# Kernel tuning notes

Measured on AMD Instinct MI355X. Metric: run time of the kernel, lower is better.

## Reference

```python
import jax, jax.numpy as jnp
import numpy as np

N, FEATURES, CODES, PAGES = 32768, 768, 64, 8192
BETA = 0.25


def _normalise(x):
    return x / jnp.linalg.norm(x, axis=-1, keepdims=True)


def setup_inputs() -> dict:
    key = jax.random.key(0)
    k_z, k_wi, k_wo, k_cb = jax.random.split(key, 4)
    return {
        "z": jax.random.normal(k_z, (N, FEATURES), dtype=jnp.float32),
        "w_in": jax.random.normal(k_wi, (CODES, FEATURES), dtype=jnp.float32) * 0.02,
        "b_in": jnp.zeros((CODES,), dtype=jnp.float32),
        "w_out": jax.random.normal(k_wo, (FEATURES, CODES), dtype=jnp.float32) * 0.02,
        "b_out": jnp.zeros((FEATURES,), dtype=jnp.float32),
        "codebook": jax.random.normal(k_cb, (PAGES, CODES), dtype=jnp.float32),
    }


def reference(z, w_in, b_in, w_out, b_out, codebook):
    sg = jax.lax.stop_gradient
    # project + L2-normalise samples and codes
    zq = _normalise(z @ w_in.T + b_in)          # [n, codes]
    cn = _normalise(codebook)                   # [pages, codes]
    # squared euclidean distance without materialising [n, pages, codes]:
    # ||z||^2 + ||c||^2 - 2 z c^T
    d = (
        jnp.sum(zq * zq, axis=-1, keepdims=True)
        + jnp.sum(cn * cn, axis=-1)[None, :]
        - 2.0 * (zq @ cn.T)
    )                                           # [n, pages]
    idxes = jnp.argmin(d, axis=-1)              # [n]
    codes = _normalise(codebook[idxes])         # lookup then normalise, as in source
    loss = BETA * jnp.mean((sg(zq) - codes) ** 2) + jnp.mean((zq - sg(codes)) ** 2)
    codes = zq + sg(codes - zq)                 # straight-through
    out = codes @ w_out.T + b_out               # [n, features]
    return out, loss, idxes
```

## Files before the change

### kernel.cpp

```cpp
#include <hip/hip_runtime.h>

#define N 32768
#define F 768
#define C 64
#define P 8192
#define TAU 1e-3f

typedef __attribute__((ext_vector_type(8))) short short8;
typedef __attribute__((ext_vector_type(4))) float f32x4;

#define WS_CNT    0
#define WS_CC     (WS_CNT + C*P)
#define WS_ZQT    (WS_CC + P)
#define WS_CODEST (WS_ZQT + C*N)
#define WS_IDX    (WS_CODEST + C*N)
#define WS_QN     (WS_IDX + N)
#define WS_ACC    (WS_QN + 1)
#define WS_QLIST  (WS_ACC + 1)
#define WS_CNH    ((WS_QLIST + N + 3) & ~3)
#define WS_CNL    (WS_CNH + (C*P)/2)
#define WS_ZQH    (WS_CNL + (C*P)/2)
#define WS_ZQL    (WS_ZQH + (C*N)/2)
#define WS_D12    (WS_ZQL + (C*N)/2)

#define OUT_LOSS_OFF (N*F)
#define OUT_IDX_OFF  (N*F + 1)

__device__ inline unsigned short f2bf(float x) {
    union { float f; unsigned u; } v; v.f = x;
    unsigned r = v.u + 0x7fffu + ((v.u >> 16) & 1u);
    return (unsigned short)(r >> 16);
}
__device__ inline float bf2f(unsigned short b) {
    union { unsigned u; float f; } v; v.u = ((unsigned)b) << 16;
    return v.f;
}

__global__ __launch_bounds__(256) void k1_norm_codebook(
    const float* __restrict__ cb, float* __restrict__ cnT, float* __restrict__ cc,
    unsigned short* __restrict__ cnh, unsigned short* __restrict__ cnl) {
    int p = blockIdx.x * 256 + threadIdx.x;
    const float4* cb4 = (const float4*)(cb + (size_t)p * C);
    float4 v[16];
    float ss = 0.f;
#pragma unroll
    for (int i = 0; i < 16; ++i) {
        v[i] = cb4[i];
        ss += v[i].x * v[i].x + v[i].y * v[i].y + v[i].z * v[i].z + v[i].w * v[i].w;
    }
    float nrm = sqrtf(ss);
    float s2 = 0.f;
    unsigned short hb[64], lb[64];
#pragma unroll
    for (int i = 0; i < 16; ++i) {
        float c4[4] = {v[i].x / nrm, v[i].y / nrm, v[i].z / nrm, v[i].w / nrm};
#pragma unroll
        for (int j = 0; j < 4; ++j) {
            cnT[(size_t)(i * 4 + j) * P + p] = c4[j];
            s2 += c4[j] * c4[j];
            unsigned short h = f2bf(c4[j]);
            hb[i * 4 + j] = h;
            lb[i * 4 + j] = f2bf(c4[j] - bf2f(h));
        }
    }
    cc[p] = s2;
#pragma unroll
    for (int i = 0; i < 8; ++i) {
        uint4 hv, lv;
        hv.x = (unsigned)hb[i*8+0] | ((unsigned)hb[i*8+1] << 16);
        hv.y = (unsigned)hb[i*8+2] | ((unsigned)hb[i*8+3] << 16);
        hv.z = (unsigned)hb[i*8+4] | ((unsigned)hb[i*8+5] << 16);
        hv.w = (unsigned)hb[i*8+6] | ((unsigned)hb[i*8+7] << 16);
        lv.x = (unsigned)lb[i*8+0] | ((unsigned)lb[i*8+1] << 16);
        lv.y = (unsigned)lb[i*8+2] | ((unsigned)lb[i*8+3] << 16);
        lv.z = (unsigned)lb[i*8+4] | ((unsigned)lb[i*8+5] << 16);
        lv.w = (unsigned)lb[i*8+6] | ((unsigned)lb[i*8+7] << 16);
        *(uint4*)&cnh[(size_t)p * 64 + i * 8] = hv;
        *(uint4*)&cnl[(size_t)p * 64 + i * 8] = lv;
    }
}

__global__ __launch_bounds__(256) void k2_project(
    const float* __restrict__ z, const float* __restrict__ w_in, const float* __restrict__ b_in,
    float* __restrict__ zqT, unsigned short* __restrict__ zqh, unsigned short* __restrict__ zql) {
    __shared__ float zrow[128 * 33];
    __shared__ float wrow[64 * 32];
    __shared__ float red[128 * 9];
    int tid = threadIdx.x;
    int tr = tid & 31;
    int tc = tid >> 5;
    int rb = blockIdx.x * 128;

    float y[4][8];
#pragma unroll
    for (int i = 0; i < 4; ++i)
#pragma unroll
        for (int j = 0; j < 8; ++j) y[i][j] = 0.f;

    for (int kt = 0; kt < F; kt += 32) {
        __syncthreads();
        for (int i = tid; i < 128 * 32; i += 256) {
            int r = i >> 5, k = i & 31;
            zrow[r * 33 + k] = z[(size_t)(rb + r) * F + kt + k];
        }
        for (int i = tid; i < 64 * 32; i += 256) {
            int c = i >> 5, k = i & 31;
            wrow[c * 32 + k] = w_in[(size_t)c * F + kt + k];
        }
        __syncthreads();
#pragma unroll
        for (int k4 = 0; k4 < 8; ++k4) {
            float zs[4][4];
#pragma unroll
            for (int i = 0; i < 4; ++i)
#pragma unroll
                for (int kk = 0; kk < 4; ++kk)
                    zs[i][kk] = zrow[(tr * 4 + i) * 33 + k4 * 4 + kk];
#pragma unroll
            for (int j = 0; j < 8; ++j) {
                float4 wv = *(const float4*)&wrow[(tc * 8 + j) * 32 + k4 * 4];
#pragma unroll
                for (int i = 0; i < 4; ++i)
                    y[i][j] = fmaf(zs[i][3], wv.w,
                              fmaf(zs[i][2], wv.z,
                              fmaf(zs[i][1], wv.y,
                              fmaf(zs[i][0], wv.x, y[i][j]))));
            }
        }
    }
#pragma unroll
    for (int j = 0; j < 8; ++j) {
        float b = b_in[tc * 8 + j];
#pragma unroll
        for (int i = 0; i < 4; ++i) y[i][j] += b;
    }
    __syncthreads();
#pragma unroll
    for (int i = 0; i < 4; ++i) {
        float s = 0.f;
#pragma unroll
        for (int j = 0; j < 8; ++j) s += y[i][j] * y[i][j];
        red[(tr * 4 + i) * 9 + tc] = s;
    }
    __syncthreads();
    float nrm[4];
#pragma unroll
    for (int i = 0; i < 4; ++i) {
        float t = 0.f;
#pragma unroll
        for (int t8 = 0; t8 < 8; ++t8) t += red[(tr * 4 + i) * 9 + t8];
        nrm[i] = sqrtf(t);
    }
    float q[4][8];
#pragma unroll
    for (int i = 0; i < 4; ++i)
#pragma unroll
        for (int j = 0; j < 8; ++j) q[i][j] = y[i][j] / nrm[i];
#pragma unroll
    for (int j = 0; j < 8; ++j) {
        int c = tc * 8 + j;
        float4 o = make_float4(q[0][j], q[1][j], q[2][j], q[3][j]);
        *(float4*)&zqT[(size_t)c * N + rb + tr * 4] = o;
    }
#pragma unroll
    for (int i = 0; i < 4; ++i) {
        unsigned short h[8], l[8];
#pragma unroll
        for (int j = 0; j < 8; ++j) {
            h[j] = f2bf(q[i][j]);
            l[j] = f2bf(q[i][j] - bf2f(h[j]));
        }
        uint4 hv, lv;
        hv.x = (unsigned)h[0] | ((unsigned)h[1] << 16);
        hv.y = (unsigned)h[2] | ((unsigned)h[3] << 16);
        hv.z = (unsigned)h[4] | ((unsigned)h[5] << 16);
        hv.w = (unsigned)h[6] | ((unsigned)h[7] << 16);
        lv.x = (unsigned)l[0] | ((unsigned)l[1] << 16);
        lv.y = (unsigned)l[2] | ((unsigned)l[3] << 16);
        lv.z = (unsigned)l[4] | ((unsigned)l[5] << 16);
        lv.w = (unsigned)l[6] | ((unsigned)l[7] << 16);
        size_t ro = (size_t)(rb + tr * 4 + i) * 64 + tc * 8;
        *(uint4*)&zqh[ro] = hv;
        *(uint4*)&zql[ro] = lv;
    }
}

__global__ __launch_bounds__(256, 4) void k3_argmin_mfma(
    const unsigned short* __restrict__ zqh, const unsigned short* __restrict__ zql,
    const unsigned short* __restrict__ cnh, const unsigned short* __restrict__ cnl,
    float4* __restrict__ d12) {
    __shared__ unsigned short lfrag[8 * 4 * 64 * 8];
    int tid = threadIdx.x;
    int w = tid >> 6, lane = tid & 63;
    int col = lane & 15, quad = lane >> 4;
    int rb = (blockIdx.x & 255) * 128;
    int ph = blockIdx.x >> 8;
    int wrow = rb + w * 32;
    int p0 = ph * (P / 4);

    short8 ah[2][2], al[2][2];
#pragma unroll
    for (int mm = 0; mm < 2; ++mm)
#pragma unroll
        for (int kf = 0; kf < 2; ++kf) {
            size_t off = (size_t)(wrow + mm * 16 + col) * 64 + kf * 32 + quad * 8;
            ah[mm][kf] = *(const short8*)&zqh[off];
            al[mm][kf] = *(const short8*)&zql[off];
        }

    float s1[8], s2[8]; int i1[8];
#pragma unroll
    for (int r = 0; r < 8; ++r) { s1[r] = -3.4e38f; s2[r] = -3.4e38f; i1[r] = 0; }

    int sq = (tid >> 4) & 3, scol = tid & 15, sf = w;
    const unsigned short* ssrc = (sf & 2) ? cnl : cnh;
    int skf = sf & 1;

    for (int pt = p0; pt < p0 + P / 4; pt += 128) {
        __syncthreads();
#pragma unroll
        for (int nt = 0; nt < 8; ++nt) {
            int p = pt + nt * 16 + scol;
            uint4 dv = *(const uint4*)&ssrc[(size_t)p * 64 + skf * 32 + sq * 8];
            *(uint4*)&lfrag[((nt * 4 + sf) * 64 + (tid & 63)) * 8] = dv;
        }
        __syncthreads();
#pragma unroll 2
        for (int nt = 0; nt < 8; ++nt) {
            short8 bh0 = *(const short8*)&lfrag[((nt * 4 + 0) * 64 + lane) * 8];
            short8 bh1 = *(const short8*)&lfrag[((nt * 4 + 1) * 64 + lane) * 8];
            short8 bl0 = *(const short8*)&lfrag[((nt * 4 + 2) * 64 + lane) * 8];
            short8 bl1 = *(const short8*)&lfrag[((nt * 4 + 3) * 64 + lane) * 8];
            int p = pt + nt * 16 + col;
#pragma unroll
            for (int mm = 0; mm < 2; ++mm) {
                f32x4 acc = {0.f, 0.f, 0.f, 0.f};
                acc = __builtin_amdgcn_mfma_f32_16x16x32_bf16(ah[mm][0], bh0, acc, 0, 0, 0);
                acc = __builtin_amdgcn_mfma_f32_16x16x32_bf16(ah[mm][1], bh1, acc, 0, 0, 0);
                acc = __builtin_amdgcn_mfma_f32_16x16x32_bf16(ah[mm][0], bl0, acc, 0, 0, 0);
                acc = __builtin_amdgcn_mfma_f32_16x16x32_bf16(ah[mm][1], bl1, acc, 0, 0, 0);
                acc = __builtin_amdgcn_mfma_f32_16x16x32_bf16(al[mm][0], bh0, acc, 0, 0, 0);
                acc = __builtin_amdgcn_mfma_f32_16x16x32_bf16(al[mm][1], bh1, acc, 0, 0, 0);
#pragma unroll
                for (int s = 0; s < 4; ++s) {
                    float sv = acc[s];
                    int r = mm * 4 + s;
                    bool gt = sv > s1[r];
                    i1[r] = gt ? p : i1[r];
                    s2[r] = fmaxf(s2[r], fminf(s1[r], sv));
                    s1[r] = fmaxf(s1[r], sv);
                }
            }
        }
    }
#pragma unroll
    for (int r = 0; r < 8; ++r) {
        float a1v = s1[r], a2v = s2[r]; int ai = i1[r];
#pragma unroll
        for (int m = 1; m <= 8; m <<= 1) {
            float b1 = __shfl_xor(a1v, m); int bi = __shfl_xor(ai, m);
            float b2 = __shfl_xor(a2v, m);
            float n1 = fmaxf(a1v, b1);
            a2v = fmaxf(fminf(a1v, b1), fmaxf(a2v, b2));
            ai = (b1 > a1v) ? bi : ai;
            a1v = n1;
        }
        if (col == 0) {
            int row = wrow + (r >> 2) * 16 + quad * 4 + (r & 3);
            d12[ph * N + row] = make_float4(a1v, a2v, __int_as_float(ai), 0.f);
        }
    }
}

__global__ __launch_bounds__(256) void k3m_merge(
    const float4* __restrict__ d12, int* __restrict__ idx_ws, float* __restrict__ idx_out,
    int* __restrict__ qn, int* __restrict__ qlist) {
    int row = blockIdx.x * 256 + threadIdx.x;
    float4 a = d12[row];
    float m1 = a.x, m2 = a.y; int i1 = __float_as_int(a.z);
#pragma unroll
    for (int ph = 1; ph < 4; ++ph) {
        float4 b = d12[ph * N + row];
        m2 = fmaxf(fminf(m1, b.x), fmaxf(m2, b.y));
        if (b.x > m1) { i1 = __float_as_int(b.z); m1 = b.x; }
    }
    idx_ws[row] = i1;
    idx_out[row] = (float)i1;
    if (m1 - m2 < 0.5f * TAU + 2e-6f) {
        int qi = atomicAdd(qn, 1);
        qlist[qi] = row;
    }
}

__global__ __launch_bounds__(256) void k3_recheck(
    const float* __restrict__ zqT, const float* __restrict__ cnT,
    const float* __restrict__ cc, const int* __restrict__ qn,
    const int* __restrict__ qlist, int* __restrict__ idx_ws, float* __restrict__ idx_out) {
    __shared__ float zrow[64];
    __shared__ float bv[4];
    __shared__ int   bi4[4];
    int tid = threadIdx.x, w = tid >> 6, lane = tid & 63;
    int nq = qn[0];
    for (int e = blockIdx.x; e < nq; e += gridDim.x) {
        int row = qlist[e];
        __syncthreads();
        if (tid < 64) zrow[tid] = zqT[(size_t)tid * N + row];
        __syncthreads();
        float best = 3.4e38f; int bp = 0;
        for (int pb = w * 2048; pb < (w + 1) * 2048; pb += 64) {
            int p = pb + lane;
            float a0 = 0.f, a1 = 0.f, a2 = 0.f, a3 = 0.f;
#pragma unroll
            for (int k = 0; k < 64; k += 4) {
                a0 = fmaf(zrow[k + 0], cnT[(size_t)(k + 0) * P + p], a0);
                a1 = fmaf(zrow[k + 1], cnT[(size_t)(k + 1) * P + p], a1);
                a2 = fmaf(zrow[k + 2], cnT[(size_t)(k + 2) * P + p], a2);
                a3 = fmaf(zrow[k + 3], cnT[(size_t)(k + 3) * P + p], a3);
            }
            float d = fmaf((a0 + a1) + (a2 + a3), -2.0f, cc[p]);
            if (d < best) { best = d; bp = p; }
        }
#pragma unroll
        for (int m = 1; m < 64; m <<= 1) {
            float ob = __shfl_xor(best, m); int op = __shfl_xor(bp, m);
            if (ob < best || (ob == best && op < bp)) { best = ob; bp = op; }
        }
        if (lane == 0) { bv[w] = best; bi4[w] = bp; }
        __syncthreads();
        if (tid == 0) {
            float b = bv[0]; int pi = bi4[0];
#pragma unroll
            for (int ww = 1; ww < 4; ++ww)
                if (bv[ww] < b || (bv[ww] == b && bi4[ww] < pi)) { b = bv[ww]; pi = bi4[ww]; }
            idx_ws[row] = pi; idx_out[row] = (float)pi;
        }
    }
}

__global__ __launch_bounds__(256) void k3b_gather(
    const float* __restrict__ cnT, const int* __restrict__ idx, float* __restrict__ codesT) {
    for (size_t i = (size_t)blockIdx.x * 256 + threadIdx.x; i < (size_t)C * N;
         i += (size_t)gridDim.x * 256) {
        int k = (int)(i >> 15);
        int r = (int)(i & (N - 1));
        codesT[i] = cnT[(size_t)k * P + idx[r]];
    }
}

__global__ __launch_bounds__(256) void k4_out(
    const float* __restrict__ codesT, const float* __restrict__ w_out,
    const float* __restrict__ b_out, float* __restrict__ out) {
    __shared__ float cds[64 * 64];
    __shared__ float wo[64 * 65];
    int tid = threadIdx.x;
    int tx = tid & 15;
    int ty = tid >> 4;
    int rb = blockIdx.x * 64;

    for (int i = tid; i < 64 * 64; i += 256) {
        int k = i >> 6, r = i & 63;
        cds[k * 64 + r] = codesT[(size_t)k * N + rb + r];
    }
    for (int ft = 0; ft < F; ft += 64) {
        __syncthreads();
        for (int i = tid; i < 64 * 64; i += 256) {
            int k = i & 63, f = i >> 6;
            wo[k * 65 + f] = w_out[(size_t)(ft + f) * C + k];
        }
        __syncthreads();
        float acc[4][4];
#pragma unroll
        for (int i = 0; i < 4; ++i)
#pragma unroll
            for (int j = 0; j < 4; ++j) acc[i][j] = 0.f;
#pragma unroll 8
        for (int k = 0; k < 64; ++k) {
            float4 cf = *(const float4*)&cds[k * 64 + ty * 4];
            float cr[4] = {cf.x, cf.y, cf.z, cf.w};
            float wv[4];
#pragma unroll
            for (int j = 0; j < 4; ++j) wv[j] = wo[k * 65 + tx * 4 + j];
#pragma unroll
            for (int i = 0; i < 4; ++i)
#pragma unroll
                for (int j = 0; j < 4; ++j)
                    acc[i][j] = fmaf(cr[i], wv[j], acc[i][j]);
        }
#pragma unroll
        for (int i = 0; i < 4; ++i) {
            int r = rb + ty * 4 + i;
            float4 o;
            o.x = acc[i][0] + b_out[ft + tx * 4 + 0];
            o.y = acc[i][1] + b_out[ft + tx * 4 + 1];
            o.z = acc[i][2] + b_out[ft + tx * 4 + 2];
            o.w = acc[i][3] + b_out[ft + tx * 4 + 3];
            *(float4*)&out[(size_t)r * F + ft + tx * 4] = o;
        }
    }
}

__global__ __launch_bounds__(256) void k5_loss(
    const float* __restrict__ zqT, const float* __restrict__ codesT, float* __restrict__ acc) {
    float s = 0.f;
    for (size_t i = (size_t)blockIdx.x * 256 + threadIdx.x; i < (size_t)C * N;
         i += (size_t)gridDim.x * 256) {
        float d = zqT[i] - codesT[i];
        s = fmaf(d, d, s);
    }
#pragma unroll
    for (int off = 32; off > 0; off >>= 1) s += __shfl_xor(s, off);
    __shared__ float wsum[4];
    int lane = threadIdx.x & 63, wv = threadIdx.x >> 6;
    if (lane == 0) wsum[wv] = s;
    __syncthreads();
    if (threadIdx.x == 0) atomicAdd(acc, wsum[0] + wsum[1] + wsum[2] + wsum[3]);
}

__global__ void k6_finalize(const float* __restrict__ acc, float* __restrict__ loss_out) {
    float m = acc[0] / (float)(C * N);
    loss_out[0] = 0.25f * m + m;
}

extern "C" void kernel_launch(void* const* d_in, const int* in_sizes, int n_in,
                              void* d_out, int out_size, void* d_ws, size_t ws_size,
                              hipStream_t stream) {
    const float* z      = (const float*)d_in[0];
    const float* w_in   = (const float*)d_in[1];
    const float* b_in   = (const float*)d_in[2];
    const float* w_out  = (const float*)d_in[3];
    const float* b_out  = (const float*)d_in[4];
    const float* cb     = (const float*)d_in[5];
    float* out = (float*)d_out;
    float* ws  = (float*)d_ws;

    unsigned short* cnh = (unsigned short*)(ws + WS_CNH);
    unsigned short* cnl = (unsigned short*)(ws + WS_CNL);
    unsigned short* zqh = (unsigned short*)(ws + WS_ZQH);
    unsigned short* zql = (unsigned short*)(ws + WS_ZQL);

    hipMemsetAsync(ws + WS_QN, 0, 2 * sizeof(float), stream);
    k1_norm_codebook<<<P / 256, 256, 0, stream>>>(cb, ws + WS_CNT, ws + WS_CC, cnh, cnl);
    k2_project<<<N / 128, 256, 0, stream>>>(z, w_in, b_in, ws + WS_ZQT, zqh, zql);
    k3_argmin_mfma<<<1024, 256, 0, stream>>>(zqh, zql, cnh, cnl, (float4*)(ws + WS_D12));
    k3m_merge<<<N / 256, 256, 0, stream>>>((const float4*)(ws + WS_D12),
                                           (int*)(ws + WS_IDX), out + OUT_IDX_OFF,
                                           (int*)(ws + WS_QN), (int*)(ws + WS_QLIST));
    k3_recheck<<<512, 256, 0, stream>>>(ws + WS_ZQT, ws + WS_CNT, ws + WS_CC,
                                        (const int*)(ws + WS_QN), (const int*)(ws + WS_QLIST),
                                        (int*)(ws + WS_IDX), out + OUT_IDX_OFF);
    k3b_gather<<<2048, 256, 0, stream>>>(ws + WS_CNT, (const int*)(ws + WS_IDX), ws + WS_CODEST);
    k4_out<<<N / 64, 256, 0, stream>>>(ws + WS_CODEST, w_out, b_out, out);
    k5_loss<<<2048, 256, 0, stream>>>(ws + WS_ZQT, ws + WS_CODEST, ws + WS_ACC);
    k6_finalize<<<1, 1, 0, stream>>>(ws + WS_ACC, out + OUT_LOSS_OFF);
}
```

Measured before the change: 621.7 us.

## Use split-bf16 MFMA for output projection, fuse gather into loss, retile projection

The output projection now gathers normalised codebook rows straight from the split-bf16 codebook by index and runs bf16 MFMA with a hi/lo split (three products) instead of an fp32 LDS-tiled GEMM. The gather and loss kernels are fused so the codesT intermediate is never written or re-read. The input projection kernel moves to 64-row blocks with a strided row mapping. This removes an intermediate buffer pass and uses matrix cores for the large write-bound output stage, at the cost of split-bf16 rounding error and uncoalesced per-element output stores.

```diff
diff --git a/kernel.cpp b/kernel.cpp
--- a/kernel.cpp
+++ b/kernel.cpp
@@ -22,6 +22,8 @@
 #define WS_ZQH    (WS_CNL + (C*P)/2)
 #define WS_ZQL    (WS_ZQH + (C*N)/2)
 #define WS_D12    (WS_ZQL + (C*N)/2)
+#define WS_WOH    (WS_D12 + 16*N)
+#define WS_WOL    (WS_WOH + (F*C)/2)
 
 #define OUT_LOSS_OFF (N*F)
 #define OUT_IDX_OFF  (N*F + 1)
@@ -83,23 +85,23 @@
 __global__ __launch_bounds__(256) void k2_project(
     const float* __restrict__ z, const float* __restrict__ w_in, const float* __restrict__ b_in,
     float* __restrict__ zqT, unsigned short* __restrict__ zqh, unsigned short* __restrict__ zql) {
-    __shared__ float zrow[128 * 33];
+    __shared__ float zrow[64 * 33];
     __shared__ float wrow[64 * 32];
-    __shared__ float red[128 * 9];
+    __shared__ float red[64 * 9];
     int tid = threadIdx.x;
     int tr = tid & 31;
     int tc = tid >> 5;
-    int rb = blockIdx.x * 128;
-
-    float y[4][8];
-#pragma unroll
-    for (int i = 0; i < 4; ++i)
+    int rb = blockIdx.x * 64;
+
+    float y[2][8];
+#pragma unroll
+    for (int i = 0; i < 2; ++i)
 #pragma unroll
         for (int j = 0; j < 8; ++j) y[i][j] = 0.f;
 
     for (int kt = 0; kt < F; kt += 32) {
         __syncthreads();
-        for (int i = tid; i < 128 * 32; i += 256) {
+        for (int i = tid; i < 64 * 32; i += 256) {
             int r = i >> 5, k = i & 31;
             zrow[r * 33 + k] = z[(size_t)(rb + r) * F + kt + k];
         }
@@ -110,17 +112,17 @@
         __syncthreads();
 #pragma unroll
         for (int k4 = 0; k4 < 8; ++k4) {
-            float zs[4][4];
-#pragma unroll
-            for (int i = 0; i < 4; ++i)
+            float zs[2][4];
+#pragma unroll
+            for (int i = 0; i < 2; ++i)
 #pragma unroll
                 for (int kk = 0; kk < 4; ++kk)
-                    zs[i][kk] = zrow[(tr * 4 + i) * 33 + k4 * 4 + kk];
+                    zs[i][kk] = zrow[(tr + 32 * i) * 33 + k4 * 4 + kk];
 #pragma unroll
             for (int j = 0; j < 8; ++j) {
                 float4 wv = *(const float4*)&wrow[(tc * 8 + j) * 32 + k4 * 4];
 #pragma unroll
-                for (int i = 0; i < 4; ++i)
+                for (int i = 0; i < 2; ++i)
                     y[i][j] = fmaf(zs[i][3], wv.w,
                               fmaf(zs[i][2], wv.z,
                               fmaf(zs[i][1], wv.y,
@@ -132,38 +134,39 @@
     for (int j = 0; j < 8; ++j) {
         float b = b_in[tc * 8 + j];
 #pragma unroll
-        for (int i = 0; i < 4; ++i) y[i][j] += b;
+        for (int i = 0; i < 2; ++i) y[i][j] += b;
     }
     __syncthreads();
 #pragma unroll
-    for (int i = 0; i < 4; ++i) {
+    for (int i = 0; i < 2; ++i) {
         float s = 0.f;
 #pragma unroll
         for (int j = 0; j < 8; ++j) s += y[i][j] * y[i][j];
-        red[(tr * 4 + i) * 9 + tc] = s;
+        red[(tr + 32 * i) * 9 + tc] = s;
     }
     __syncthreads();
-    float nrm[4];
-#pragma unroll
-    for (int i = 0; i < 4; ++i) {
+    float nrm[2];
+#pragma unroll
+    for (int i = 0; i < 2; ++i) {
         float t = 0.f;
 #pragma unroll
-        for (int t8 = 0; t8 < 8; ++t8) t += red[(tr * 4 + i) * 9 + t8];
+        for (int t8 = 0; t8 < 8; ++t8) t += red[(tr + 32 * i) * 9 + t8];
         nrm[i] = sqrtf(t);
     }
-    float q[4][8];
-#pragma unroll
-    for (int i = 0; i < 4; ++i)
+    float q[2][8];
+#pragma unroll
+    for (int i = 0; i < 2; ++i)
 #pragma unroll
         for (int j = 0; j < 8; ++j) q[i][j] = y[i][j] / nrm[i];
 #pragma unroll
     for (int j = 0; j < 8; ++j) {
         int c = tc * 8 + j;
-        float4 o = make_float4(q[0][j], q[1][j], q[2][j], q[3][j]);
-        *(float4*)&zqT[(size_t)c * N + rb + tr * 4] = o;
-    }
-#pragma unroll
-    for (int i = 0; i < 4; ++i) {
+#pragma unroll
+        for (int i = 0; i < 2; ++i)
+            zqT[(size_t)c * N + rb + tr + 32 * i] = q[i][j];
+    }
+#pragma unroll
+    for (int i = 0; i < 2; ++i) {
         unsigned short h[8], l[8];
 #pragma unroll
         for (int j = 0; j < 8; ++j) {
@@ -179,7 +182,7 @@
         lv.y = (unsigned)l[2] | ((unsigned)l[3] << 16);
         lv.z = (unsigned)l[4] | ((unsigned)l[5] << 16);
         lv.w = (unsigned)l[6] | ((unsigned)l[7] << 16);
-        size_t ro = (size_t)(rb + tr * 4 + i) * 64 + tc * 8;
+        size_t ro = (size_t)(rb + tr + 32 * i) * 64 + tc * 8;
         *(uint4*)&zqh[ro] = hv;
         *(uint4*)&zql[ro] = lv;
     }
@@ -337,74 +340,15 @@
     }
 }
 
-__global__ __launch_bounds__(256) void k3b_gather(
-    const float* __restrict__ cnT, const int* __restrict__ idx, float* __restrict__ codesT) {
+__global__ __launch_bounds__(256) void k3b_gather_loss(
+    const float* __restrict__ cnT, const int* __restrict__ idx,
+    const float* __restrict__ zqT, float* __restrict__ acc) {
+    float s = 0.f;
     for (size_t i = (size_t)blockIdx.x * 256 + threadIdx.x; i < (size_t)C * N;
          i += (size_t)gridDim.x * 256) {
         int k = (int)(i >> 15);
         int r = (int)(i & (N - 1));
-        codesT[i] = cnT[(size_t)k * P + idx[r]];
-    }
-}
-
-__global__ __launch_bounds__(256) void k4_out(
-    const float* __restrict__ codesT, const float* __restrict__ w_out,
-    const float* __restrict__ b_out, float* __restrict__ out) {
-    __shared__ float cds[64 * 64];
-    __shared__ float wo[64 * 65];
-    int tid = threadIdx.x;
-    int tx = tid & 15;
-    int ty = tid >> 4;
-    int rb = blockIdx.x * 64;
-
-    for (int i = tid; i < 64 * 64; i += 256) {
-        int k = i >> 6, r = i & 63;
-        cds[k * 64 + r] = codesT[(size_t)k * N + rb + r];
-    }
-    for (int ft = 0; ft < F; ft += 64) {
-        __syncthreads();
-        for (int i = tid; i < 64 * 64; i += 256) {
-            int k = i & 63, f = i >> 6;
-            wo[k * 65 + f] = w_out[(size_t)(ft + f) * C + k];
-        }
-        __syncthreads();
-        float acc[4][4];
-#pragma unroll
-        for (int i = 0; i < 4; ++i)
-#pragma unroll
-            for (int j = 0; j < 4; ++j) acc[i][j] = 0.f;
-#pragma unroll 8
-        for (int k = 0; k < 64; ++k) {
-            float4 cf = *(const float4*)&cds[k * 64 + ty * 4];
-            float cr[4] = {cf.x, cf.y, cf.z, cf.w};
-            float wv[4];
-#pragma unroll
-            for (int j = 0; j < 4; ++j) wv[j] = wo[k * 65 + tx * 4 + j];
-#pragma unroll
-            for (int i = 0; i < 4; ++i)
-#pragma unroll
-                for (int j = 0; j < 4; ++j)
-                    acc[i][j] = fmaf(cr[i], wv[j], acc[i][j]);
-        }
-#pragma unroll
-        for (int i = 0; i < 4; ++i) {
-            int r = rb + ty * 4 + i;
-            float4 o;
-            o.x = acc[i][0] + b_out[ft + tx * 4 + 0];
-            o.y = acc[i][1] + b_out[ft + tx * 4 + 1];
-            o.z = acc[i][2] + b_out[ft + tx * 4 + 2];
-            o.w = acc[i][3] + b_out[ft + tx * 4 + 3];
-            *(float4*)&out[(size_t)r * F + ft + tx * 4] = o;
-        }
-    }
-}
-
-__global__ __launch_bounds__(256) void k5_loss(
-    const float* __restrict__ zqT, const float* __restrict__ codesT, float* __restrict__ acc) {
-    float s = 0.f;
-    for (size_t i = (size_t)blockIdx.x * 256 + threadIdx.x; i < (size_t)C * N;
-         i += (size_t)gridDim.x * 256) {
-        float d = zqT[i] - codesT[i];
+        float d = zqT[i] - cnT[(size_t)k * P + idx[r]];
         s = fmaf(d, d, s);
     }
 #pragma unroll
@@ -414,6 +358,57 @@
     if (lane == 0) wsum[wv] = s;
     __syncthreads();
     if (threadIdx.x == 0) atomicAdd(acc, wsum[0] + wsum[1] + wsum[2] + wsum[3]);
+}
+
+__global__ __launch_bounds__(256) void k4_prep(
+    const float* __restrict__ w_out, unsigned short* __restrict__ woh,
+    unsigned short* __restrict__ wol) {
+    int i = blockIdx.x * 256 + threadIdx.x;
+    float v = w_out[i];
+    unsigned short h = f2bf(v);
+    woh[i] = h;
+    wol[i] = f2bf(v - bf2f(h));
+}
+
+__global__ __launch_bounds__(256) void k4_out_mfma(
+    const unsigned short* __restrict__ cnh, const unsigned short* __restrict__ cnl,
+    const unsigned short* __restrict__ woh, const unsigned short* __restrict__ wol,
+    const int* __restrict__ idx, const float* __restrict__ b_out, float* __restrict__ out) {
+    int tid = threadIdx.x;
+    int w = tid >> 6, lane = tid & 63;
+    int col = lane & 15, quad = lane >> 4;
+    int rb = (blockIdx.x >> 2) * 64;
+    int fb = (blockIdx.x & 3) * 192;
+    int wrow = rb + w * 16;
+
+    int pg = idx[wrow + col];
+    short8 ah[2], al[2];
+#pragma unroll
+    for (int kf = 0; kf < 2; ++kf) {
+        size_t off = (size_t)pg * 64 + kf * 32 + quad * 8;
+        ah[kf] = *(const short8*)&cnh[off];
+        al[kf] = *(const short8*)&cnl[off];
+    }
+
+    for (int ft = 0; ft < 12; ++ft) {
+        int f0 = fb + ft * 16;
+        size_t bo = (size_t)(f0 + col) * 64 + quad * 8;
+        short8 bh0 = *(const short8*)&woh[bo];
+        short8 bh1 = *(const short8*)&woh[bo + 32];
+        short8 bl0 = *(const short8*)&wol[bo];
+        short8 bl1 = *(const short8*)&wol[bo + 32];
+        f32x4 acc = {0.f, 0.f, 0.f, 0.f};
+        acc = __builtin_amdgcn_mfma_f32_16x16x32_bf16(ah[0], bh0, acc, 0, 0, 0);
+        acc = __builtin_amdgcn_mfma_f32_16x16x32_bf16(ah[1], bh1, acc, 0, 0, 0);
+        acc = __builtin_amdgcn_mfma_f32_16x16x32_bf16(ah[0], bl0, acc, 0, 0, 0);
+        acc = __builtin_amdgcn_mfma_f32_16x16x32_bf16(ah[1], bl1, acc, 0, 0, 0);
+        acc = __builtin_amdgcn_mfma_f32_16x16x32_bf16(al[0], bh0, acc, 0, 0, 0);
+        acc = __builtin_amdgcn_mfma_f32_16x16x32_bf16(al[1], bh1, acc, 0, 0, 0);
+        float bv = b_out[f0 + col];
+#pragma unroll
+        for (int s = 0; s < 4; ++s)
+            out[(size_t)(wrow + quad * 4 + s) * F + f0 + col] = acc[s] + bv;
+    }
 }
 
 __global__ void k6_finalize(const float* __restrict__ acc, float* __restrict__ loss_out) {
@@ -437,10 +432,13 @@
     unsigned short* cnl = (unsigned short*)(ws + WS_CNL);
     unsigned short* zqh = (unsigned short*)(ws + WS_ZQH);
     unsigned short* zql = (unsigned short*)(ws + WS_ZQL);
+    unsigned short* woh = (unsigned short*)(ws + WS_WOH);
+    unsigned short* wol = (unsigned short*)(ws + WS_WOL);
 
     hipMemsetAsync(ws + WS_QN, 0, 2 * sizeof(float), stream);
     k1_norm_codebook<<<P / 256, 256, 0, stream>>>(cb, ws + WS_CNT, ws + WS_CC, cnh, cnl);
-    k2_project<<<N / 128, 256, 0, stream>>>(z, w_in, b_in, ws + WS_ZQT, zqh, zql);
+    k4_prep<<<F * C / 256, 256, 0, stream>>>(w_out, woh, wol);
+    k2_project<<<N / 64, 256, 0, stream>>>(z, w_in, b_in, ws + WS_ZQT, zqh, zql);
     k3_argmin_mfma<<<1024, 256, 0, stream>>>(zqh, zql, cnh, cnl, (float4*)(ws + WS_D12));
     k3m_merge<<<N / 256, 256, 0, stream>>>((const float4*)(ws + WS_D12),
                                            (int*)(ws + WS_IDX), out + OUT_IDX_OFF,
@@ -448,8 +446,9 @@
     k3_recheck<<<512, 256, 0, stream>>>(ws + WS_ZQT, ws + WS_CNT, ws + WS_CC,
                                         (const int*)(ws + WS_QN), (const int*)(ws + WS_QLIST),
                                         (int*)(ws + WS_IDX), out + OUT_IDX_OFF);
-    k3b_gather<<<2048, 256, 0, stream>>>(ws + WS_CNT, (const int*)(ws + WS_IDX), ws + WS_CODEST);
-    k4_out<<<N / 64, 256, 0, stream>>>(ws + WS_CODEST, w_out, b_out, out);
-    k5_loss<<<2048, 256, 0, stream>>>(ws + WS_ZQT, ws + WS_CODEST, ws + WS_ACC);
+    k3b_gather_loss<<<2048, 256, 0, stream>>>(ws + WS_CNT, (const int*)(ws + WS_IDX),
+                                              ws + WS_ZQT, ws + WS_ACC);
+    k4_out_mfma<<<2048, 256, 0, stream>>>(cnh, cnl, woh, wol, (const int*)(ws + WS_IDX),
+                                          b_out, out);
     k6_finalize<<<1, 1, 0, stream>>>(ws + WS_ACC, out + OUT_LOSS_OFF);
 }
```

Result: no change. 614.1 us (-1.2%).
